# Performance work log

Hardware: AMD Instinct MI355X
Metric: run time of the kernel (lower is better)

Reference implementation:

```python
import jax, jax.numpy as jnp
import numpy as np

B, C, H, W = 4, 512, 64, 64          # visual feature map
NTXT, TDIM, HEADS = 256, 1024, 8     # context tokens, textual dim, heads
DHEAD = TDIM // HEADS


def setup_inputs() -> dict:
    key = jax.random.key(0)
    ks = jax.random.split(key, 8)
    x = jax.random.normal(ks[0], (B, C, H, W), dtype=jnp.float32)
    timesteps = jax.random.randint(ks[1], (B,), 0, 1000)
    context = jax.random.normal(ks[2], (B, NTXT, TDIM), dtype=jnp.float32)
    # Linear weights stored as (in, out) so y = x @ W (matches torch x @ W.T)
    s = 0.02
    Wq = jax.random.normal(ks[3], (TDIM, TDIM), dtype=jnp.float32) * s
    Wk = jax.random.normal(ks[4], (C, TDIM), dtype=jnp.float32) * s
    Wv = jax.random.normal(ks[5], (C, TDIM), dtype=jnp.float32) * s
    Wo = jax.random.normal(ks[6], (TDIM, TDIM), dtype=jnp.float32) * s
    bo = jnp.zeros((TDIM,), dtype=jnp.float32)
    return {"x": x, "timesteps": timesteps, "context": context,
            "Wq": Wq, "Wk": Wk, "Wv": Wv, "Wo": Wo, "bo": bo}


def reference(x, timesteps, context, Wq, Wk, Wv, Wo, bo):
    b, c, h, w = x.shape
    # b c h w -> b (h w) c
    vis = x.reshape(b, c, h * w).transpose(0, 2, 1)
    q = context @ Wq                       # [b, ntxt, tdim]
    k = vis @ Wk                           # [b, hw, tdim]
    v = vis @ Wv                           # [b, hw, tdim]
    def split_heads(t):
        bb, n, _ = t.shape
        return t.reshape(bb, n, HEADS, DHEAD).transpose(0, 2, 1, 3)  # b h n d
    q, k, v = map(split_heads, (q, k, v))
    scale = DHEAD ** -0.5
    sim = jnp.einsum('bhid,bhjd->bhij', q, k) * scale   # [b,h,ntxt,hw]
    attn = jax.nn.softmax(sim, axis=-1)
    out = jnp.einsum('bhij,bhjd->bhid', attn, v)        # [b,h,ntxt,d]
    out = out.transpose(0, 2, 1, 3).reshape(b, -1, TDIM)  # b n (h d)
    return out @ Wo + bo                                  # dropout p=0 is identity
```

## Files before the change

kernel.cpp:

```cpp
#include <hip/hip_runtime.h>

typedef __attribute__((ext_vector_type(8))) short short8;
typedef __attribute__((ext_vector_type(4))) float f32x4;
typedef __attribute__((ext_vector_type(4))) int int4v;

#define DEV static __device__ __forceinline__

DEV float bf2f(unsigned short u) { return __uint_as_float(((unsigned)u) << 16); }
DEV unsigned short f2bf(float f) {
  unsigned u = __float_as_uint(f);
  u = (u + 0x7FFFu + ((u >> 16) & 1u)) >> 16;
  return (unsigned short)u;
}

DEV void gload_lds16(const void* g, void* l) {
  __builtin_amdgcn_global_load_lds(
      (const __attribute__((address_space(1))) void*)g,
      (__attribute__((address_space(3))) void*)l, 16, 0, 0);
}

__global__ __launch_bounds__(256) void k_cast_bf16(const float* __restrict__ in,
                                                   unsigned short* __restrict__ out) {
  long i = ((long)blockIdx.x * 256 + threadIdx.x) * 4;
  float4 v = *(const float4*)(in + i);
  ushort4 o;
  o.x = f2bf(v.x); o.y = f2bf(v.y); o.z = f2bf(v.z); o.w = f2bf(v.w);
  *(ushort4*)(out + i) = o;
}

__global__ __launch_bounds__(256) void k_transpose_cast(const float* __restrict__ in,
                                                        unsigned short* __restrict__ out,
                                                        int R, int Cc, long sInZ, long sOutZ) {
  __shared__ float t[32][33];
  long zi = (long)blockIdx.z * sInZ, zo = (long)blockIdx.z * sOutZ;
  int c0 = blockIdx.x * 32, r0 = blockIdx.y * 32;
  int tx = threadIdx.x & 31, ty = threadIdx.x >> 5;
#pragma unroll
  for (int i = 0; i < 4; ++i)
    t[ty + 8 * i][tx] = in[zi + (long)(r0 + ty + 8 * i) * Cc + c0 + tx];
  __syncthreads();
#pragma unroll
  for (int i = 0; i < 4; ++i)
    out[zo + (long)(c0 + ty + 8 * i) * R + r0 + tx] = f2bf(t[tx][ty + 8 * i]);
}

__global__ __launch_bounds__(256) void k_gemm(
    const unsigned short* __restrict__ A, const unsigned short* __restrict__ B,
    void* __restrict__ Cout, const float* __restrict__ bias,
    int K, int lda, int ldb, int ldc,
    long sAb, long sAh, long sBb, long sBh, long sCb, long sCh, int epi) {
  __shared__ __align__(16) char lds[32768];
  char* As = lds;
  char* Bs = lds + 16384;
  int z = blockIdx.z, zb = z >> 3, zh = z & 7;
  const unsigned short* Ab = A + (long)zb * sAb + (long)zh * sAh;
  const unsigned short* Bb = B + (long)zb * sBb + (long)zh * sBh;
  int tid = threadIdx.x;
  int m0 = blockIdx.x * 128, n0 = blockIdx.y * 128;
  int lane = tid & 63, wid = tid >> 6;
  int wm = (wid >> 1) * 64, wn = (wid & 1) * 64;
  int l15 = lane & 15, lg = lane >> 4;

  f32x4 acc[4][4];
#pragma unroll
  for (int i = 0; i < 4; ++i)
#pragma unroll
    for (int j = 0; j < 4; ++j)
      acc[i][j] = (f32x4){0.f, 0.f, 0.f, 0.f};

  for (int k0 = 0; k0 < K; k0 += 64) {
    __syncthreads();
#pragma unroll
    for (int p = 0; p < 4; ++p) {
      int r = (wid * 4 + p) * 8 + (lane >> 3);
      int cs8 = ((lane & 7) ^ (r & 7)) * 8;
      gload_lds16(Ab + (long)(m0 + r) * lda + k0 + cs8, As + (wid * 4 + p) * 1024);
      gload_lds16(Bb + (long)(n0 + r) * ldb + k0 + cs8, Bs + (wid * 4 + p) * 1024);
    }
    __syncthreads();
#pragma unroll
    for (int ks = 0; ks < 2; ++ks) {
      short8 af[4], bfr[4];
#pragma unroll
      for (int t = 0; t < 4; ++t) {
        int mr = wm + t * 16 + l15;
        af[t] = *(const short8*)(As + mr * 128 + (((lg * 16) + ks * 64) ^ ((mr & 7) << 4)));
        int nr = wn + t * 16 + l15;
        bfr[t] = *(const short8*)(Bs + nr * 128 + (((lg * 16) + ks * 64) ^ ((nr & 7) << 4)));
      }
#pragma unroll
      for (int mt = 0; mt < 4; ++mt)
#pragma unroll
        for (int nt = 0; nt < 4; ++nt)
          acc[mt][nt] = __builtin_amdgcn_mfma_f32_16x16x32_bf16(af[mt], bfr[nt], acc[mt][nt], 0, 0, 0);
    }
  }

  long cbase = (long)zb * sCb + (long)zh * sCh;
#pragma unroll
  for (int mt = 0; mt < 4; ++mt) {
#pragma unroll
    for (int r = 0; r < 4; ++r) {
      long row = m0 + wm + mt * 16 + lg * 4 + r;
      long rowoff = cbase + row * (long)ldc;
#pragma unroll
      for (int nt = 0; nt < 4; ++nt) {
        int col = n0 + wn + nt * 16 + l15;
        float v = acc[mt][nt][r];
        if (epi == 0)
          ((unsigned short*)Cout)[rowoff + col] = f2bf(v);
        else
          ((float*)Cout)[rowoff + col] = v + bias[col];
      }
    }
  }
}

__global__ __launch_bounds__(256) void k_transpose_v(const unsigned short* __restrict__ KV,
                                                     unsigned short* __restrict__ Vt) {
  __shared__ __align__(16) char tl[64 * 144];
  int b = blockIdx.z;
  int t0 = blockIdx.x * 64;
  int h0 = blockIdx.y * 64;
  int g = threadIdx.x & 7, r = threadIdx.x >> 3;
  const unsigned short* src = KV + (long)b * 4096 * 2048 + 1024;
#pragma unroll
  for (int p = 0; p < 2; ++p) {
    int hw = r + 32 * p;
    short8 vv = *(const short8*)(src + (long)(h0 + hw) * 2048 + t0 + g * 8);
    *(short8*)(tl + hw * 144 + ((g * 16) ^ (((hw >> 3) & 7) << 4))) = vv;
  }
  __syncthreads();
  unsigned short* dst = Vt + (long)b * 1024 * 4096;
#pragma unroll
  for (int p = 0; p < 2; ++p) {
    int tr = r + 32 * p;
    short8 ov;
#pragma unroll
    for (int j = 0; j < 8; ++j) {
      int hw = g * 8 + j;
      ov[j] = *(const short*)(tl + hw * 144 + ((tr * 2) ^ (((hw >> 3) & 7) << 4)));
    }
    *(short8*)(dst + (long)(t0 + tr) * 4096 + h0 + g * 8) = ov;
  }
}

__global__ __launch_bounds__(512) void k_flash(
    const unsigned short* __restrict__ Qb, const unsigned short* __restrict__ KV,
    const unsigned short* __restrict__ Vt, float* __restrict__ Po,
    float* __restrict__ Pm, float* __restrict__ Pl) {
  __shared__ __align__(16) char lds[81920];
  char* Ks = lds;
  char* Vs = lds + 32768;
  char* Ps = lds + 65536;
  int qt = blockIdx.x, sp = blockIdx.y, bh = blockIdx.z;
  int b = bh >> 3, h = bh & 7;
  int tid = threadIdx.x, lane = tid & 63, wid = tid >> 6;
  int l15 = lane & 15, lg = lane >> 4;
  const float cs = 0.08838834764831845f * 1.4426950408889634f;

  const unsigned short* kvb = KV + (long)b * 4096 * 2048 + h * 128;
  const unsigned short* vtb = Vt + (long)b * 1024 * 4096 + (long)h * 128 * 4096;

  int qrow = qt * 128 + wid * 16 + l15;
  const unsigned short* qp = Qb + ((long)(b * 256 + qrow)) * 1024 + h * 128;
  short8 qf[4];
#pragma unroll
  for (int dt = 0; dt < 4; ++dt)
    qf[dt] = *(const short8*)(qp + dt * 32 + lg * 8);

  f32x4 acc_o[8];
#pragma unroll
  for (int i = 0; i < 8; ++i) acc_o[i] = (f32x4){0.f, 0.f, 0.f, 0.f};
  float m_r[4], l_r[4];
#pragma unroll
  for (int r = 0; r < 4; ++r) { m_r[r] = -1e30f; l_r[r] = 0.f; }

  char* pw = Ps + wid * 2048;
  int krK = lane >> 4, kcK = lane & 15;
  int krV = lane >> 3, kcV = lane & 7;

  auto stage = [&](int it, int buf) {
    int kv0 = sp * 512 + it * 64;
    char* kb = Ks + (buf << 14);
    char* vb = Vs + (buf << 14);
#pragma unroll
    for (int p = 0; p < 2; ++p) {
      int seg = wid * 2 + p;
      int r = seg * 4 + krK;
      gload_lds16(kvb + (long)(kv0 + r) * 2048 + ((kcK ^ (r & 7)) * 8), kb + seg * 1024);
      int d = seg * 8 + krV;
      gload_lds16(vtb + (long)d * 4096 + kv0 + ((kcV ^ (d & 7)) * 8), vb + seg * 1024);
    }
  };

  stage(0, 0);
  __syncthreads();
  int cur = 0;

  for (int it = 0; it < 8; ++it) {
    if (it + 1 < 8) stage(it + 1, cur ^ 1);
    const char* Kc = Ks + (cur << 14);
    const char* Vc = Vs + (cur << 14);

    f32x4 s[4];
#pragma unroll
    for (int t = 0; t < 4; ++t) s[t] = (f32x4){0.f, 0.f, 0.f, 0.f};
#pragma unroll
    for (int t = 0; t < 4; ++t) {
      int krow = t * 16 + l15;
#pragma unroll
      for (int dt = 0; dt < 4; ++dt) {
        short8 kf = *(const short8*)(Kc + krow * 256 + ((dt * 64 + lg * 16) ^ ((krow & 7) << 4)));
        s[t] = __builtin_amdgcn_mfma_f32_16x16x32_bf16(qf[dt], kf, s[t], 0, 0, 0);
      }
    }

    float pm[4];
#pragma unroll
    for (int r = 0; r < 4; ++r)
      pm[r] = fmaxf(fmaxf(s[0][r], s[1][r]), fmaxf(s[2][r], s[3][r])) * cs;
#pragma unroll
    for (int o = 1; o < 16; o <<= 1)
#pragma unroll
      for (int r = 0; r < 4; ++r) pm[r] = fmaxf(pm[r], __shfl_xor(pm[r], o));
    float cf[4], rs[4];
#pragma unroll
    for (int r = 0; r < 4; ++r) {
      float mn = fmaxf(m_r[r], pm[r]);
      cf[r] = exp2f(m_r[r] - mn);
      m_r[r] = mn;
      rs[r] = 0.f;
    }
#pragma unroll
    for (int t = 0; t < 4; ++t) {
#pragma unroll
      for (int r = 0; r < 4; ++r) {
        float p = exp2f(s[t][r] * cs - m_r[r]);
        rs[r] += p;
        int q = lg * 4 + r;
        *(unsigned short*)(pw + q * 128 + ((t * 32 + l15 * 2) ^ ((q & 7) << 4))) = f2bf(p);
      }
    }
#pragma unroll
    for (int o = 1; o < 16; o <<= 1)
#pragma unroll
      for (int r = 0; r < 4; ++r) rs[r] += __shfl_xor(rs[r], o);
#pragma unroll
    for (int r = 0; r < 4; ++r) l_r[r] = l_r[r] * cf[r] + rs[r];
#pragma unroll
    for (int dt = 0; dt < 8; ++dt)
#pragma unroll
      for (int r = 0; r < 4; ++r) acc_o[dt][r] *= cf[r];

    short8 pa0 = *(const short8*)(pw + l15 * 128 + ((lg * 16) ^ ((l15 & 7) << 4)));
    short8 pa1 = *(const short8*)(pw + l15 * 128 + ((64 + lg * 16) ^ ((l15 & 7) << 4)));
#pragma unroll
    for (int dt = 0; dt < 8; ++dt) {
      int vrow = dt * 16 + l15;
      short8 vb0 = *(const short8*)(Vc + vrow * 128 + ((lg * 16) ^ ((vrow & 7) << 4)));
      short8 vb1 = *(const short8*)(Vc + vrow * 128 + ((64 + lg * 16) ^ ((vrow & 7) << 4)));
      acc_o[dt] = __builtin_amdgcn_mfma_f32_16x16x32_bf16(pa0, vb0, acc_o[dt], 0, 0, 0);
      acc_o[dt] = __builtin_amdgcn_mfma_f32_16x16x32_bf16(pa1, vb1, acc_o[dt], 0, 0, 0);
    }
    __syncthreads();
    cur ^= 1;
  }

  int qbase = qt * 128 + wid * 16;
  long pobase = (long)((sp * 32 + bh) * 256) * 128;
#pragma unroll
  for (int dt = 0; dt < 8; ++dt)
#pragma unroll
    for (int r = 0; r < 4; ++r) {
      int q = qbase + lg * 4 + r;
      Po[pobase + (long)q * 128 + dt * 16 + l15] = acc_o[dt][r];
    }
  if (l15 == 0) {
#pragma unroll
    for (int r = 0; r < 4; ++r) {
      int q = qbase + lg * 4 + r;
      Pm[(sp * 32 + bh) * 256 + q] = m_r[r];
      Pl[(sp * 32 + bh) * 256 + q] = l_r[r];
    }
  }
}

__global__ __launch_bounds__(256) void k_combine(const float* __restrict__ Po,
                                                 const float* __restrict__ Pm,
                                                 const float* __restrict__ Pl,
                                                 unsigned short* __restrict__ AOut) {
  int gid = blockIdx.x * 256 + threadIdx.x;
  int row = gid >> 5, dg = gid & 31;
  int bh = row >> 8, q = row & 255;
  int b = bh >> 3, h = bh & 7;
  int mi = bh * 256 + q;
  const int ms = 32 * 256;
  float m[8];
  float mx = -1e30f;
#pragma unroll
  for (int s = 0; s < 8; ++s) { m[s] = Pm[s * ms + mi]; mx = fmaxf(mx, m[s]); }
  float wgt[8];
  float denom = 0.f;
#pragma unroll
  for (int s = 0; s < 8; ++s) {
    wgt[s] = exp2f(m[s] - mx);
    denom += Pl[s * ms + mi] * wgt[s];
  }
  float inv = 1.f / denom;
  long base = (long)row * 128 + dg * 4;
  const long stride = (long)32 * 256 * 128;
  f32x4 acc = (f32x4){0.f, 0.f, 0.f, 0.f};
#pragma unroll
  for (int s = 0; s < 8; ++s) {
    f32x4 o = *(const f32x4*)(Po + base + s * stride);
#pragma unroll
    for (int i = 0; i < 4; ++i) acc[i] += o[i] * wgt[s];
  }
  ushort4 res;
#pragma unroll
  for (int i = 0; i < 4; ++i) ((unsigned short*)&res)[i] = f2bf(acc[i] * inv);
  *(ushort4*)(AOut + ((long)(b * 256 + q)) * 1024 + h * 128 + dg * 4) = res;
}

extern "C" void kernel_launch(void* const* d_in, const int* in_sizes, int n_in,
                              void* d_out, int out_size, void* d_ws, size_t ws_size,
                              hipStream_t stream) {
  const float* x   = (const float*)d_in[0];
  const float* ctx = (const float*)d_in[2];
  const float* Wq  = (const float*)d_in[3];
  const float* Wk  = (const float*)d_in[4];
  const float* Wv  = (const float*)d_in[5];
  const float* Wo  = (const float*)d_in[6];
  const float* bo  = (const float*)d_in[7];
  float* out = (float*)d_out;

  char* w = (char*)d_ws;
  auto alloc = [&](long bytes) { char* p = w; w += (bytes + 255) & ~255L; return p; };
  unsigned short* xT   = (unsigned short*)alloc((long)4 * 4096 * 512 * 2);
  unsigned short* WqT  = (unsigned short*)alloc((long)1024 * 1024 * 2);
  unsigned short* WkvT = (unsigned short*)alloc((long)2048 * 512 * 2);
  unsigned short* WoT  = (unsigned short*)alloc((long)1024 * 1024 * 2);
  unsigned short* ctxb = (unsigned short*)alloc((long)4 * 256 * 1024 * 2);
  unsigned short* Qb   = (unsigned short*)alloc((long)4 * 256 * 1024 * 2);
  unsigned short* KV   = (unsigned short*)alloc((long)4 * 4096 * 2048 * 2);
  unsigned short* Vt   = (unsigned short*)alloc((long)4 * 1024 * 4096 * 2);
  float*          Po   = (float*)alloc((long)8 * 32 * 256 * 128 * 4);
  float*          Pm   = (float*)alloc((long)8 * 32 * 256 * 4);
  float*          Pl   = (float*)alloc((long)8 * 32 * 256 * 4);
  unsigned short* AOut = (unsigned short*)alloc((long)4 * 256 * 1024 * 2);

  k_cast_bf16<<<1024, 256, 0, stream>>>(ctx, ctxb);
  k_transpose_cast<<<dim3(32, 32, 1), 256, 0, stream>>>(Wq, WqT, 1024, 1024, 0, 0);
  k_transpose_cast<<<dim3(32, 16, 1), 256, 0, stream>>>(Wk, WkvT, 512, 1024, 0, 0);
  k_transpose_cast<<<dim3(32, 16, 1), 256, 0, stream>>>(Wv, WkvT + 1024 * 512, 512, 1024, 0, 0);
  k_transpose_cast<<<dim3(32, 32, 1), 256, 0, stream>>>(Wo, WoT, 1024, 1024, 0, 0);
  k_transpose_cast<<<dim3(128, 16, 4), 256, 0, stream>>>(x, xT, 512, 4096,
                                                         (long)512 * 4096, (long)4096 * 512);

  k_gemm<<<dim3(8, 8, 1), 256, 0, stream>>>(ctxb, WqT, Qb, nullptr,
      1024, 1024, 1024, 1024, 0, 0, 0, 0, 0, 0, 0);
  k_gemm<<<dim3(128, 16, 1), 256, 0, stream>>>(xT, WkvT, KV, nullptr,
      512, 512, 512, 2048, 0, 0, 0, 0, 0, 0, 0);
  k_transpose_v<<<dim3(16, 64, 4), 256, 0, stream>>>(KV, Vt);
  k_flash<<<dim3(2, 8, 32), 512, 0, stream>>>(Qb, KV, Vt, Po, Pm, Pl);
  k_combine<<<1024, 256, 0, stream>>>(Po, Pm, Pl, AOut);
  k_gemm<<<dim3(8, 8, 1), 256, 0, stream>>>(AOut, WoT, out, bo,
      1024, 1024, 1024, 1024, 0, 0, 0, 0, 0, 0, 1);
}
```

Before: 272.0 us.

## Compute V transposed directly via swapped GEMM and store flash partials in bf16

The fused K/V projection is split in two. K is written into its own buffer, and V^T is produced directly by a batched GEMM that swaps the operands (WvT times xT). This removes the separate k_transpose_v pass and its extra read and write of V. The flash kernel now normalizes each split's partial output by its own l and stores it as bf16, and the combine step weights the splits by l·exp. This halves partial-output traffic at the cost of some precision in the intermediate partials.

```diff
diff --git a/kernel.cpp b/kernel.cpp
--- a/kernel.cpp
+++ b/kernel.cpp
@@ -116,38 +116,9 @@
   }
 }
 
-__global__ __launch_bounds__(256) void k_transpose_v(const unsigned short* __restrict__ KV,
-                                                     unsigned short* __restrict__ Vt) {
-  __shared__ __align__(16) char tl[64 * 144];
-  int b = blockIdx.z;
-  int t0 = blockIdx.x * 64;
-  int h0 = blockIdx.y * 64;
-  int g = threadIdx.x & 7, r = threadIdx.x >> 3;
-  const unsigned short* src = KV + (long)b * 4096 * 2048 + 1024;
-#pragma unroll
-  for (int p = 0; p < 2; ++p) {
-    int hw = r + 32 * p;
-    short8 vv = *(const short8*)(src + (long)(h0 + hw) * 2048 + t0 + g * 8);
-    *(short8*)(tl + hw * 144 + ((g * 16) ^ (((hw >> 3) & 7) << 4))) = vv;
-  }
-  __syncthreads();
-  unsigned short* dst = Vt + (long)b * 1024 * 4096;
-#pragma unroll
-  for (int p = 0; p < 2; ++p) {
-    int tr = r + 32 * p;
-    short8 ov;
-#pragma unroll
-    for (int j = 0; j < 8; ++j) {
-      int hw = g * 8 + j;
-      ov[j] = *(const short*)(tl + hw * 144 + ((tr * 2) ^ (((hw >> 3) & 7) << 4)));
-    }
-    *(short8*)(dst + (long)(t0 + tr) * 4096 + h0 + g * 8) = ov;
-  }
-}
-
 __global__ __launch_bounds__(512) void k_flash(
-    const unsigned short* __restrict__ Qb, const unsigned short* __restrict__ KV,
-    const unsigned short* __restrict__ Vt, float* __restrict__ Po,
+    const unsigned short* __restrict__ Qb, const unsigned short* __restrict__ Kb,
+    const unsigned short* __restrict__ Vt, unsigned short* __restrict__ Po,
     float* __restrict__ Pm, float* __restrict__ Pl) {
   __shared__ __align__(16) char lds[81920];
   char* Ks = lds;
@@ -159,7 +130,7 @@
   int l15 = lane & 15, lg = lane >> 4;
   const float cs = 0.08838834764831845f * 1.4426950408889634f;
 
-  const unsigned short* kvb = KV + (long)b * 4096 * 2048 + h * 128;
+  const unsigned short* kvb = Kb + (long)b * 4096 * 1024 + h * 128;
   const unsigned short* vtb = Vt + (long)b * 1024 * 4096 + (long)h * 128 * 4096;
 
   int qrow = qt * 128 + wid * 16 + l15;
@@ -188,7 +159,7 @@
     for (int p = 0; p < 2; ++p) {
       int seg = wid * 2 + p;
       int r = seg * 4 + krK;
-      gload_lds16(kvb + (long)(kv0 + r) * 2048 + ((kcK ^ (r & 7)) * 8), kb + seg * 1024);
+      gload_lds16(kvb + (long)(kv0 + r) * 1024 + ((kcK ^ (r & 7)) * 8), kb + seg * 1024);
       int d = seg * 8 + krV;
       gload_lds16(vtb + (long)d * 4096 + kv0 + ((kcV ^ (d & 7)) * 8), vb + seg * 1024);
     }
@@ -267,6 +238,9 @@
     cur ^= 1;
   }
 
+  float invl[4];
+#pragma unroll
+  for (int r = 0; r < 4; ++r) invl[r] = 1.f / l_r[r];
   int qbase = qt * 128 + wid * 16;
   long pobase = (long)((sp * 32 + bh) * 256) * 128;
 #pragma unroll
@@ -274,7 +248,7 @@
 #pragma unroll
     for (int r = 0; r < 4; ++r) {
       int q = qbase + lg * 4 + r;
-      Po[pobase + (long)q * 128 + dt * 16 + l15] = acc_o[dt][r];
+      Po[pobase + (long)q * 128 + dt * 16 + l15] = f2bf(acc_o[dt][r] * invl[r]);
     }
   if (l15 == 0) {
 #pragma unroll
@@ -286,7 +260,7 @@
   }
 }
 
-__global__ __launch_bounds__(256) void k_combine(const float* __restrict__ Po,
+__global__ __launch_bounds__(256) void k_combine(const unsigned short* __restrict__ Po,
                                                  const float* __restrict__ Pm,
                                                  const float* __restrict__ Pl,
                                                  unsigned short* __restrict__ AOut) {
@@ -304,8 +278,8 @@
   float denom = 0.f;
 #pragma unroll
   for (int s = 0; s < 8; ++s) {
-    wgt[s] = exp2f(m[s] - mx);
-    denom += Pl[s * ms + mi] * wgt[s];
+    wgt[s] = Pl[s * ms + mi] * exp2f(m[s] - mx);
+    denom += wgt[s];
   }
   float inv = 1.f / denom;
   long base = (long)row * 128 + dg * 4;
@@ -313,9 +287,11 @@
   f32x4 acc = (f32x4){0.f, 0.f, 0.f, 0.f};
 #pragma unroll
   for (int s = 0; s < 8; ++s) {
-    f32x4 o = *(const f32x4*)(Po + base + s * stride);
-#pragma unroll
-    for (int i = 0; i < 4; ++i) acc[i] += o[i] * wgt[s];
+    ushort4 o = *(const ushort4*)(Po + base + s * stride);
+    acc[0] += bf2f(o.x) * wgt[s];
+    acc[1] += bf2f(o.y) * wgt[s];
+    acc[2] += bf2f(o.z) * wgt[s];
+    acc[3] += bf2f(o.w) * wgt[s];
   }
   ushort4 res;
 #pragma unroll
@@ -339,31 +315,34 @@
   auto alloc = [&](long bytes) { char* p = w; w += (bytes + 255) & ~255L; return p; };
   unsigned short* xT   = (unsigned short*)alloc((long)4 * 4096 * 512 * 2);
   unsigned short* WqT  = (unsigned short*)alloc((long)1024 * 1024 * 2);
-  unsigned short* WkvT = (unsigned short*)alloc((long)2048 * 512 * 2);
+  unsigned short* WkT  = (unsigned short*)alloc((long)1024 * 512 * 2);
+  unsigned short* WvT  = (unsigned short*)alloc((long)1024 * 512 * 2);
   unsigned short* WoT  = (unsigned short*)alloc((long)1024 * 1024 * 2);
   unsigned short* ctxb = (unsigned short*)alloc((long)4 * 256 * 1024 * 2);
   unsigned short* Qb   = (unsigned short*)alloc((long)4 * 256 * 1024 * 2);
-  unsigned short* KV   = (unsigned short*)alloc((long)4 * 4096 * 2048 * 2);
+  unsigned short* Kb   = (unsigned short*)alloc((long)4 * 4096 * 1024 * 2);
   unsigned short* Vt   = (unsigned short*)alloc((long)4 * 1024 * 4096 * 2);
-  float*          Po   = (float*)alloc((long)8 * 32 * 256 * 128 * 4);
+  unsigned short* Po   = (unsigned short*)alloc((long)8 * 32 * 256 * 128 * 2);
   float*          Pm   = (float*)alloc((long)8 * 32 * 256 * 4);
   float*          Pl   = (float*)alloc((long)8 * 32 * 256 * 4);
   unsigned short* AOut = (unsigned short*)alloc((long)4 * 256 * 1024 * 2);
 
   k_cast_bf16<<<1024, 256, 0, stream>>>(ctx, ctxb);
   k_transpose_cast<<<dim3(32, 32, 1), 256, 0, stream>>>(Wq, WqT, 1024, 1024, 0, 0);
-  k_transpose_cast<<<dim3(32, 16, 1), 256, 0, stream>>>(Wk, WkvT, 512, 1024, 0, 0);
-  k_transpose_cast<<<dim3(32, 16, 1), 256, 0, stream>>>(Wv, WkvT + 1024 * 512, 512, 1024, 0, 0);
+  k_transpose_cast<<<dim3(32, 16, 1), 256, 0, stream>>>(Wk, WkT, 512, 1024, 0, 0);
+  k_transpose_cast<<<dim3(32, 16, 1), 256, 0, stream>>>(Wv, WvT, 512, 1024, 0, 0);
   k_transpose_cast<<<dim3(32, 32, 1), 256, 0, stream>>>(Wo, WoT, 1024, 1024, 0, 0);
   k_transpose_cast<<<dim3(128, 16, 4), 256, 0, stream>>>(x, xT, 512, 4096,
                                                          (long)512 * 4096, (long)4096 * 512);
 
   k_gemm<<<dim3(8, 8, 1), 256, 0, stream>>>(ctxb, WqT, Qb, nullptr,
       1024, 1024, 1024, 1024, 0, 0, 0, 0, 0, 0, 0);
-  k_gemm<<<dim3(128, 16, 1), 256, 0, stream>>>(xT, WkvT, KV, nullptr,
-      512, 512, 512, 2048, 0, 0, 0, 0, 0, 0, 0);
-  k_transpose_v<<<dim3(16, 64, 4), 256, 0, stream>>>(KV, Vt);
-  k_flash<<<dim3(2, 8, 32), 512, 0, stream>>>(Qb, KV, Vt, Po, Pm, Pl);
+  k_gemm<<<dim3(128, 8, 1), 256, 0, stream>>>(xT, WkT, Kb, nullptr,
+      512, 512, 512, 1024, 0, 0, 0, 0, 0, 0, 0);
+  k_gemm<<<dim3(8, 32, 4), 256, 0, stream>>>(WvT, xT, Vt, nullptr,
+      512, 512, 512, 4096,
+      0, 0, 0, (long)4096 * 512, 0, (long)1024 * 4096, 0);
+  k_flash<<<dim3(2, 8, 32), 512, 0, stream>>>(Qb, Kb, Vt, Po, Pm, Pl);
   k_combine<<<1024, 256, 0, stream>>>(Po, Pm, Pl, AOut);
   k_gemm<<<dim3(8, 8, 1), 256, 0, stream>>>(AOut, WoT, out, bo,
       1024, 1024, 1024, 1024, 0, 0, 0, 0, 0, 0, 1);
```

Result: faster. 265.8 us (-2.3%).
